# Kernel optimization log

Hardware: AMD Instinct MI355X
Metric: run time of the kernel (lower is better)

Reference implementation:

```python
import jax, jax.numpy as jnp
import numpy as np

B_SZ, SEQ, IN, HID, MEM_D, ORDER = 64, 512, 512, 1024, 8, 256
THETA = 512.0


def _legendre_ab(order, theta):
    # Continuous-time Legendre delay system (Voelker et al.):
    # A[i,j] = (2i+1)/theta * (-1 if i<j else (-1)^(i-j+1));  B[i] = (2i+1)/theta * (-1)^i
    q = jnp.arange(order, dtype=jnp.float32)
    r = (2.0 * q + 1.0) / theta
    i, j = jnp.meshgrid(q, q, indexing='ij')
    a = jnp.where(i < j, -1.0, jnp.where(((i - j) % 2) == 1, 1.0, -1.0)) * r[:, None]
    b = jnp.where((q % 2) == 0, 1.0, -1.0) * r
    # ZOH discretization with dt=1 via augmented matrix exponential
    M = jnp.zeros((order + 1, order + 1), dtype=jnp.float32)
    M = M.at[:order, :order].set(a).at[:order, order].set(b)
    Md = jax.scipy.linalg.expm(M)
    return Md[:order, :order], Md[:order, order]


def setup_inputs() -> dict:
    key = jax.random.key(0)
    ks = jax.random.split(key, 7)
    def n(k, shape, s):
        return jax.random.normal(k, shape, dtype=jnp.float32) * jnp.float32(s)
    return {
        'x':   n(ks[0], (B_SZ, SEQ, IN), 1.0),
        'e_x': n(ks[1], (MEM_D, IN), 1.0 / np.sqrt(IN)),          # lecun_uniform_-like scale
        'e_h': n(ks[2], (MEM_D, HID), 1.0 / np.sqrt(HID)),
        'e_m': jnp.zeros((MEM_D, MEM_D * ORDER), dtype=jnp.float32),  # init_em = zeros_
        'W_x': n(ks[4], (HID, IN), np.sqrt(2.0 / (HID + IN))),    # xavier_normal_
        'W_h': n(ks[5], (HID, HID), np.sqrt(2.0 / (HID + HID))),
        'W_m': n(ks[6], (HID, MEM_D * ORDER), np.sqrt(2.0 / (HID + MEM_D * ORDER))),
    }


def reference(x, e_x, e_h, e_m, W_x, W_h, W_m):
    A, Bv = _legendre_ab(ORDER, THETA)
    bsz = x.shape[0]

    def step(carry, x_t):
        h, m = carry                      # h: [B,HID], m: [B,MEM_D,ORDER]
        m_flat = m.reshape(bsz, -1)
        # u_t = e_x x_t + e_h h_{t-1} + e_m m_{t-1}  -> [B, MEM_D]
        u = x_t @ e_x.T + h @ e_h.T + m_flat @ e_m.T
        # m_t = A m_{t-1} + B u_t (per memory channel)
        m = jnp.einsum('bdo,po->bdp', m, A) + u[:, :, None] * Bv
        m_flat = m.reshape(bsz, -1)
        # h_t = tanh(W_x x_t + W_h h_{t-1} + W_m m_t)
        h = jnp.tanh(x_t @ W_x.T + h @ W_h.T + m_flat @ W_m.T)
        return (h, m), h

    h0 = jnp.zeros((bsz, HID), dtype=x.dtype)
    m0 = jnp.zeros((bsz, MEM_D, ORDER), dtype=x.dtype)
    (_, _), ys = jax.lax.scan(step, (h0, m0), jnp.swapaxes(x, 0, 1))
    return jnp.swapaxes(ys, 0, 1)          # [B, SEQ, HID]
```

## Files before the change

kernel.cpp:

```cpp
#include <hip/hip_runtime.h>
#include <cmath>
#include <vector>

#define B_SZ 64
#define SEQ 512
#define IN_D 512
#define HID 1024
#define MEM_DIM 8
#define ORD 256
#define MFLAT 2048
#define KTOT 3584
#define NH 128
#define NM 64
#define NBLK (NH + NM)
#define BAR_STRIDE 16

typedef __attribute__((ext_vector_type(8))) short short8v;
typedef __attribute__((ext_vector_type(4))) float f32x4;

__device__ __host__ inline unsigned short f2bf(float f) {
  union { float f; unsigned u; } v; v.f = f;
  unsigned r = v.u + 0x7FFF + ((v.u >> 16) & 1);
  return (unsigned short)(r >> 16);
}
__device__ __host__ inline float bf2f(unsigned short h) {
  union { unsigned u; float f; } v; v.u = ((unsigned)h) << 16;
  return v.f;
}

static void matmul_d(const double* A, const double* B, double* C, int n) {
  for (int i = 0; i < n; ++i) {
    double* Ci = C + (size_t)i * n;
    for (int j = 0; j < n; ++j) Ci[j] = 0.0;
    const double* Ai = A + (size_t)i * n;
    for (int k = 0; k < n; ++k) {
      double a = Ai[k];
      const double* Bk = B + (size_t)k * n;
      for (int j = 0; j < n; ++j) Ci[j] += a * Bk[j];
    }
  }
}

static void compute_AB_host(float* AdT, float* Anat, float* Bd) {
  const int q = ORD, n = ORD + 1;
  const double theta = 512.0;
  std::vector<double> M((size_t)n * n, 0.0);
  for (int i = 0; i < q; ++i) {
    double r = (2.0 * i + 1.0) / theta;
    for (int j = 0; j < q; ++j) {
      double v = (i < j) ? -1.0 : ((((i - j) % 2) == 1) ? 1.0 : -1.0);
      M[(size_t)i * n + j] = v * r;
    }
    M[(size_t)i * n + q] = (((i % 2) == 0) ? 1.0 : -1.0) * r;
  }
  double norm = 0.0;
  for (int j = 0; j < n; ++j) {
    double s = 0.0;
    for (int i = 0; i < n; ++i) s += fabs(M[(size_t)i * n + j]);
    if (s > norm) norm = s;
  }
  int s = 0;
  while (norm > 0.25) { norm *= 0.5; ++s; }
  double sc = ldexp(1.0, -s);
  for (size_t i = 0; i < M.size(); ++i) M[i] *= sc;
  std::vector<double> E((size_t)n * n, 0.0), P = M, T((size_t)n * n);
  for (int i = 0; i < n; ++i) E[(size_t)i * n + i] = 1.0;
  for (size_t i = 0; i < M.size(); ++i) E[i] += M[i];
  for (int k = 2; k <= 30; ++k) {
    matmul_d(P.data(), M.data(), T.data(), n);
    double inv = 1.0 / (double)k, mx = 0.0;
    for (size_t i = 0; i < T.size(); ++i) {
      T[i] *= inv;
      double a = fabs(T[i]);
      if (a > mx) mx = a;
    }
    P.swap(T);
    for (size_t i = 0; i < M.size(); ++i) E[i] += P[i];
    if (mx < 1e-19) break;
  }
  for (int it = 0; it < s; ++it) {
    matmul_d(E.data(), E.data(), T.data(), n);
    E.swap(T);
  }
  for (int p = 0; p < q; ++p) {
    for (int o = 0; o < q; ++o) {
      float v = (float)E[(size_t)p * n + o];
      AdT[(size_t)o * q + p] = v;
      Anat[(size_t)p * q + o] = v;
    }
    Bd[p] = (float)E[(size_t)p * n + q];
  }
}

__global__ __launch_bounds__(256) void k_wmb(const float* __restrict__ Wm,
                                             const float* __restrict__ Bd,
                                             float* __restrict__ WmB) {
  int i = blockIdx.x;
  int d = threadIdx.x >> 5, l = threadIdx.x & 31;
  const float* wr = Wm + (size_t)i * MFLAT + d * ORD;
  float acc = 0.f;
  #pragma unroll
  for (int j = 0; j < 8; ++j) { int p = l + 32 * j; acc += wr[p] * Bd[p]; }
  for (int off = 16; off; off >>= 1) acc += __shfl_xor(acc, off);
  if (l == 0) WmB[i * 8 + d] = acc;
}

__global__ __launch_bounds__(256) void k_gcat(
    const float* __restrict__ Wx, const float* __restrict__ Wh,
    const float* __restrict__ Wm, const float* __restrict__ Ex,
    const float* __restrict__ Eh, const float* __restrict__ Em,
    const float* __restrict__ Anat, const float* __restrict__ WmB,
    unsigned short* __restrict__ Ghi, unsigned short* __restrict__ Glo) {
  __shared__ float wm[MFLAT];
  __shared__ float wb[8];
  int i = blockIdx.x, tid = threadIdx.x;
  for (int k = tid; k < MFLAT; k += 256) wm[k] = Wm[(size_t)i * MFLAT + k];
  if (tid < 8) wb[tid] = WmB[i * 8 + tid];
  __syncthreads();
  unsigned short* grh = Ghi + (size_t)i * KTOT;
  unsigned short* grl = Glo + (size_t)i * KTOT;
  for (int c = tid; c < KTOT; c += 256) {
    float v;
    if (c < IN_D) {
      v = Wx[(size_t)i * IN_D + c];
      #pragma unroll
      for (int d = 0; d < 8; ++d) v += wb[d] * Ex[(size_t)d * IN_D + c];
    } else if (c < IN_D + HID) {
      int j = c - IN_D;
      v = Wh[(size_t)i * HID + j];
      #pragma unroll
      for (int d = 0; d < 8; ++d) v += wb[d] * Eh[(size_t)d * HID + j];
    } else {
      int cm = c - IN_D - HID;
      int dd = cm >> 8, o = cm & 255;
      v = 0.f;
      const float* wmd = wm + dd * ORD;
      for (int p = 0; p < ORD; ++p) v += wmd[p] * Anat[(size_t)p * ORD + o];
      #pragma unroll
      for (int d = 0; d < 8; ++d) v += wb[d] * Em[(size_t)d * MFLAT + cm];
    }
    unsigned short hi = f2bf(v);
    grh[c] = hi;
    grl[c] = f2bf(v - bf2f(hi));
  }
}

__device__ inline void grid_barrier(unsigned* __restrict__ arr,
                                    unsigned* __restrict__ go, unsigned ep) {
  __syncthreads();
  if (blockIdx.x == 0) {
    int tid = threadIdx.x;
    if (tid > 0 && tid < NBLK) {
      while (__hip_atomic_load(&arr[tid * BAR_STRIDE], __ATOMIC_RELAXED,
                               __HIP_MEMORY_SCOPE_AGENT) < ep) {}
    }
    __syncthreads();
    if (tid == 0)
      __hip_atomic_store(go, ep, __ATOMIC_RELEASE, __HIP_MEMORY_SCOPE_AGENT);
  } else {
    if (threadIdx.x == 0) {
      __hip_atomic_store(&arr[blockIdx.x * BAR_STRIDE], ep, __ATOMIC_RELEASE,
                         __HIP_MEMORY_SCOPE_AGENT);
      while (__hip_atomic_load(go, __ATOMIC_RELAXED,
                               __HIP_MEMORY_SCOPE_AGENT) < ep) {}
    }
  }
  if (threadIdx.x == 0)
    __builtin_amdgcn_fence(__ATOMIC_ACQUIRE, "agent");
  __syncthreads();
}

__global__ __launch_bounds__(256) void k_persist(
    const float* __restrict__ x, const float* __restrict__ Ex,
    const float* __restrict__ Eh, const float* __restrict__ Em,
    const unsigned short* __restrict__ Ghi, const unsigned short* __restrict__ Glo,
    const float* __restrict__ AdT, const float* __restrict__ Bd,
    unsigned short* __restrict__ sh0, unsigned short* __restrict__ sh1,
    unsigned short* __restrict__ sl0, unsigned short* __restrict__ sl1,
    float* __restrict__ hfp0, float* __restrict__ hfp1,
    float* __restrict__ mfp0, float* __restrict__ mfp1,
    float* __restrict__ out, unsigned* __restrict__ barArr,
    unsigned* __restrict__ barGo) {
  int tid = threadIdx.x;
  unsigned ep = 0;

  if (blockIdx.x < NH) {
    __shared__ float hx[2][64][4];
    int it = blockIdx.x & 63, bh = blockIdx.x >> 6;
    int w = tid >> 6, lane = tid & 63;
    int tw = w & 1, kh = w >> 1;
    int b0 = bh * 32 + tw * 16;
    int i0 = it * 16;
    size_t aoff = (size_t)(b0 + (lane & 15)) * KTOT + (lane >> 4) * 8;
    const unsigned short* bh_ = Ghi + (size_t)(i0 + (lane & 15)) * KTOT + (lane >> 4) * 8;
    const unsigned short* bl_ = Glo + (size_t)(i0 + (lane & 15)) * KTOT + (lane >> 4) * 8;

    grid_barrier(barArr, barGo, ++ep);

    for (int t = 0; t < SEQ; ++t) {
      const unsigned short* ah_ = ((t & 1) ? sh1 : sh0) + aoff;
      const unsigned short* al_ = ((t & 1) ? sl1 : sl0) + aoff;
      unsigned short* snh = (t & 1) ? sh0 : sh1;
      unsigned short* snl = (t & 1) ? sl0 : sl1;
      float* hn = (t & 1) ? hfp0 : hfp1;

      f32x4 ahh = {0.f,0.f,0.f,0.f}, alh = {0.f,0.f,0.f,0.f}, ahl = {0.f,0.f,0.f,0.f};
      int kbase = kh * 1792;
      #pragma unroll 4
      for (int kk = 0; kk < 56; ++kk) {
        int k = kbase + kk * 32;
        short8v avh = *(const short8v*)(ah_ + k);
        short8v avl = *(const short8v*)(al_ + k);
        short8v bvh = *(const short8v*)(bh_ + k);
        short8v bvl = *(const short8v*)(bl_ + k);
        ahh = __builtin_amdgcn_mfma_f32_16x16x32_bf16(avh, bvh, ahh, 0, 0, 0);
        alh = __builtin_amdgcn_mfma_f32_16x16x32_bf16(avl, bvh, alh, 0, 0, 0);
        ahl = __builtin_amdgcn_mfma_f32_16x16x32_bf16(avh, bvl, ahl, 0, 0, 0);
      }
      f32x4 acc = ahh + alh + ahl;
      if (kh == 1) {
        *(f32x4*)&hx[tw][lane][0] = acc;
      }
      __syncthreads();
      if (kh == 0) {
        f32x4 o4 = *(const f32x4*)&hx[tw][lane][0];
        #pragma unroll
        for (int r = 0; r < 4; ++r) {
          float v = acc[r] + o4[r];
          float hv = tanhf(v);
          int b = b0 + (lane >> 4) * 4 + r;
          int i = i0 + (lane & 15);
          hn[(size_t)b * HID + i] = hv;
          unsigned short hi = f2bf(hv);
          snh[(size_t)b * KTOT + IN_D + i] = hi;
          snl[(size_t)b * KTOT + IN_D + i] = f2bf(hv - bf2f(hi));
          __builtin_nontemporal_store(hv, &out[((size_t)b * SEQ + t) * HID + i]);
        }
      }
      grid_barrier(barArr, barGo, ++ep);
    }
  } else {
    __shared__ float sst[KTOT];
    __shared__ float part[4][MFLAT];
    __shared__ float ush[8];
    int b = blockIdx.x - NH;
    int du = tid >> 5, lu = tid & 31;
    const float* exr = Ex + (size_t)du * IN_D;
    const float* ehr = Eh + (size_t)du * HID;
    const float* emr = Em + (size_t)du * MFLAT;
    int os = tid >> 6;
    int p0 = (tid & 63) * 4;
    int dp0 = tid * 8;
    int dr = tid >> 5;
    float bdv[8];
    #pragma unroll
    for (int j = 0; j < 8; ++j) bdv[j] = Bd[(dp0 & 255) + j];

    {
      const float* xr = x + (size_t)b * SEQ * IN_D;
      for (int k = tid; k < IN_D; k += 256) {
        float xv = xr[k];
        unsigned short hi = f2bf(xv);
        sh0[(size_t)b * KTOT + k] = hi;
        sl0[(size_t)b * KTOT + k] = f2bf(xv - bf2f(hi));
      }
    }
    grid_barrier(barArr, barGo, ++ep);

    for (int t = 0; t < SEQ; ++t) {
      const float* hc = (t & 1) ? hfp1 : hfp0;
      const float* mc = (t & 1) ? mfp1 : mfp0;
      float* mn = (t & 1) ? mfp0 : mfp1;
      unsigned short* snh = (t & 1) ? sh0 : sh1;
      unsigned short* snl = (t & 1) ? sl0 : sl1;

      const float* xrow = x + ((size_t)b * SEQ + t) * IN_D;
      #pragma unroll
      for (int j = 0; j < 14; ++j) {
        int k = tid + 256 * j;
        float v;
        if (k < IN_D) v = xrow[k];
        else if (k < IN_D + HID) v = hc[(size_t)b * HID + (k - IN_D)];
        else v = mc[(size_t)b * MFLAT + (k - IN_D - HID)];
        sst[k] = v;
      }
      __syncthreads();

      float ua = 0.f;
      #pragma unroll 4
      for (int j = 0; j < 16; ++j) { int k = lu + 32 * j; ua += exr[k] * sst[k]; }
      #pragma unroll 4
      for (int j = 0; j < 32; ++j) { int k = lu + 32 * j; ua += ehr[k] * sst[IN_D + k]; }
      #pragma unroll 4
      for (int j = 0; j < 64; ++j) { int k = lu + 32 * j; ua += emr[k] * sst[IN_D + HID + k]; }
      #pragma unroll
      for (int off = 16; off; off >>= 1) ua += __shfl_xor(ua, off);
      if (lu == 0) ush[du] = ua;
      __syncthreads();

      float acc[8][4];
      #pragma unroll
      for (int d = 0; d < 8; ++d)
        acc[d][0] = acc[d][1] = acc[d][2] = acc[d][3] = 0.f;
      const float* mbase = sst + IN_D + HID;
      #pragma unroll 4
      for (int oo = 0; oo < 64; ++oo) {
        int o = os * 64 + oo;
        float4 q = *(const float4*)(AdT + (size_t)o * ORD + p0);
        #pragma unroll
        for (int d = 0; d < 8; ++d) {
          float mv = mbase[d * ORD + o];
          acc[d][0] = fmaf(q.x, mv, acc[d][0]);
          acc[d][1] = fmaf(q.y, mv, acc[d][1]);
          acc[d][2] = fmaf(q.z, mv, acc[d][2]);
          acc[d][3] = fmaf(q.w, mv, acc[d][3]);
        }
      }
      #pragma unroll
      for (int d = 0; d < 8; ++d)
        *(float4*)&part[os][d * ORD + p0] =
            make_float4(acc[d][0], acc[d][1], acc[d][2], acc[d][3]);
      __syncthreads();

      float r[8];
      float uv = ush[dr];
      #pragma unroll
      for (int j = 0; j < 8; ++j) r[j] = bdv[j] * uv;
      #pragma unroll
      for (int s = 0; s < 4; ++s) {
        float4 v0 = *(const float4*)&part[s][dp0];
        float4 v1 = *(const float4*)&part[s][dp0 + 4];
        r[0] += v0.x; r[1] += v0.y; r[2] += v0.z; r[3] += v0.w;
        r[4] += v1.x; r[5] += v1.y; r[6] += v1.z; r[7] += v1.w;
      }
      float4* mo4 = (float4*)(mn + (size_t)b * MFLAT + dp0);
      mo4[0] = make_float4(r[0], r[1], r[2], r[3]);
      mo4[1] = make_float4(r[4], r[5], r[6], r[7]);
      unsigned short ph[8], pl[8];
      #pragma unroll
      for (int j = 0; j < 8; ++j) {
        ph[j] = f2bf(r[j]);
        pl[j] = f2bf(r[j] - bf2f(ph[j]));
      }
      size_t moff = (size_t)b * KTOT + IN_D + HID + dp0;
      *(short8v*)(snh + moff) = *(short8v*)ph;
      *(short8v*)(snl + moff) = *(short8v*)pl;

      if (t + 1 < SEQ) {
        const float* xn = x + ((size_t)b * SEQ + t + 1) * IN_D;
        for (int k = tid; k < IN_D; k += 256) {
          float xv = xn[k];
          unsigned short hi = f2bf(xv);
          snh[(size_t)b * KTOT + k] = hi;
          snl[(size_t)b * KTOT + k] = f2bf(xv - bf2f(hi));
        }
      }
      grid_barrier(barArr, barGo, ++ep);
    }
  }
}

extern "C" void kernel_launch(void* const* d_in, const int* in_sizes, int n_in,
                              void* d_out, int out_size, void* d_ws, size_t ws_size,
                              hipStream_t stream) {
  const float* x  = (const float*)d_in[0];
  const float* Ex = (const float*)d_in[1];
  const float* Eh = (const float*)d_in[2];
  const float* Em = (const float*)d_in[3];
  const float* Wx = (const float*)d_in[4];
  const float* Wh = (const float*)d_in[5];
  const float* Wm = (const float*)d_in[6];
  float* out = (float*)d_out;
  float* ws = (float*)d_ws;

  float* dAnat = ws;
  float* dAdT  = dAnat + 65536;
  float* dBd   = dAdT + 65536;
  float* dWmB  = dBd + 512;
  unsigned short* dGhi = (unsigned short*)(dWmB + 8192);
  unsigned short* dGlo = dGhi + (size_t)HID * KTOT;
  unsigned short* sh0  = dGlo + (size_t)HID * KTOT;
  unsigned short* sh1  = sh0 + (size_t)B_SZ * KTOT;
  unsigned short* sl0  = sh1 + (size_t)B_SZ * KTOT;
  unsigned short* sl1  = sl0 + (size_t)B_SZ * KTOT;
  float* hfp0 = (float*)(sl1 + (size_t)B_SZ * KTOT);
  float* hfp1 = hfp0 + B_SZ * HID;
  float* mfp0 = hfp1 + B_SZ * HID;
  float* mfp1 = mfp0 + B_SZ * MFLAT;
  unsigned* barArr = (unsigned*)(mfp1 + B_SZ * MFLAT);
  unsigned* barGo  = barArr + NBLK * BAR_STRIDE;

  static float h_AdT[ORD * ORD];
  static float h_Anat[ORD * ORD];
  static float h_Bd[ORD];
  compute_AB_host(h_AdT, h_Anat, h_Bd);
  hipMemcpyAsync(dAdT,  h_AdT,  sizeof(h_AdT),  hipMemcpyHostToDevice, stream);
  hipMemcpyAsync(dAnat, h_Anat, sizeof(h_Anat), hipMemcpyHostToDevice, stream);
  hipMemcpyAsync(dBd,   h_Bd,   sizeof(h_Bd),   hipMemcpyHostToDevice, stream);

  hipMemsetAsync(sh0, 0, (size_t)B_SZ * KTOT * sizeof(unsigned short), stream);
  hipMemsetAsync(sl0, 0, (size_t)B_SZ * KTOT * sizeof(unsigned short), stream);
  hipMemsetAsync(hfp0, 0, (size_t)B_SZ * HID * sizeof(float), stream);
  hipMemsetAsync(mfp0, 0, (size_t)B_SZ * MFLAT * sizeof(float), stream);
  hipMemsetAsync(barArr, 0, (NBLK * BAR_STRIDE + 16) * sizeof(unsigned), stream);

  k_wmb<<<dim3(HID), dim3(256), 0, stream>>>(Wm, dBd, dWmB);
  k_gcat<<<dim3(HID), dim3(256), 0, stream>>>(Wx, Wh, Wm, Ex, Eh, Em, dAnat, dWmB, dGhi, dGlo);

  k_persist<<<dim3(NBLK), dim3(256), 0, stream>>>(
      x, Ex, Eh, Em, dGhi, dGlo, dAdT, dBd, sh0, sh1, sl0, sl1,
      hfp0, hfp1, mfp0, mfp1, out, barArr, barGo);
}
```

Baseline: 19.41 ms.

## Use relaxed atomic cross-block exchange and drop fp32 hidden-state buffers

The grid barrier loses its release stores and acquire fence. Cross-block shared state is now written and read with relaxed agent-scope 64-bit atomic loads and stores, which avoids cache writeback and invalidation on every step. The h-blocks pack the hi/lo bf16 hidden values through LDS into coalesced 64-bit stores. The separate fp32 h buffer is removed, so memory blocks rebuild h from the hi+lo bf16 pair. This cuts per-step barrier and store cost, but it depends on the atomics bypassing non-coherent caches. The reconstructed h also carries a small precision change. The m fp32 buffer is still read with plain loads while no acquire fence remains, which risks reading stale data.

```diff
diff --git a/kernel.cpp b/kernel.cpp
--- a/kernel.cpp
+++ b/kernel.cpp
@@ -17,6 +17,14 @@
 
 typedef __attribute__((ext_vector_type(8))) short short8v;
 typedef __attribute__((ext_vector_type(4))) float f32x4;
+typedef unsigned long long u64;
+
+__device__ inline u64 ald(const void* p) {
+  return __hip_atomic_load((const u64*)p, __ATOMIC_RELAXED, __HIP_MEMORY_SCOPE_AGENT);
+}
+__device__ inline void ast(void* p, u64 v) {
+  __hip_atomic_store((u64*)p, v, __ATOMIC_RELAXED, __HIP_MEMORY_SCOPE_AGENT);
+}
 
 __device__ __host__ inline unsigned short f2bf(float f) {
   union { float f; unsigned u; } v; v.f = f;
@@ -156,17 +164,15 @@
     }
     __syncthreads();
     if (tid == 0)
-      __hip_atomic_store(go, ep, __ATOMIC_RELEASE, __HIP_MEMORY_SCOPE_AGENT);
+      __hip_atomic_store(go, ep, __ATOMIC_RELAXED, __HIP_MEMORY_SCOPE_AGENT);
   } else {
     if (threadIdx.x == 0) {
-      __hip_atomic_store(&arr[blockIdx.x * BAR_STRIDE], ep, __ATOMIC_RELEASE,
+      __hip_atomic_store(&arr[blockIdx.x * BAR_STRIDE], ep, __ATOMIC_RELAXED,
                          __HIP_MEMORY_SCOPE_AGENT);
       while (__hip_atomic_load(go, __ATOMIC_RELAXED,
                                __HIP_MEMORY_SCOPE_AGENT) < ep) {}
     }
   }
-  if (threadIdx.x == 0)
-    __builtin_amdgcn_fence(__ATOMIC_ACQUIRE, "agent");
   __syncthreads();
 }
 
@@ -177,7 +183,6 @@
     const float* __restrict__ AdT, const float* __restrict__ Bd,
     unsigned short* __restrict__ sh0, unsigned short* __restrict__ sh1,
     unsigned short* __restrict__ sl0, unsigned short* __restrict__ sl1,
-    float* __restrict__ hfp0, float* __restrict__ hfp1,
     float* __restrict__ mfp0, float* __restrict__ mfp1,
     float* __restrict__ out, unsigned* __restrict__ barArr,
     unsigned* __restrict__ barGo) {
@@ -186,6 +191,7 @@
 
   if (blockIdx.x < NH) {
     __shared__ float hx[2][64][4];
+    __shared__ unsigned lds_pk[32][16];
     int it = blockIdx.x & 63, bh = blockIdx.x >> 6;
     int w = tid >> 6, lane = tid & 63;
     int tw = w & 1, kh = w >> 1;
@@ -202,20 +208,20 @@
       const unsigned short* al_ = ((t & 1) ? sl1 : sl0) + aoff;
       unsigned short* snh = (t & 1) ? sh0 : sh1;
       unsigned short* snl = (t & 1) ? sl0 : sl1;
-      float* hn = (t & 1) ? hfp0 : hfp1;
 
       f32x4 ahh = {0.f,0.f,0.f,0.f}, alh = {0.f,0.f,0.f,0.f}, ahl = {0.f,0.f,0.f,0.f};
       int kbase = kh * 1792;
       #pragma unroll 4
       for (int kk = 0; kk < 56; ++kk) {
         int k = kbase + kk * 32;
-        short8v avh = *(const short8v*)(ah_ + k);
-        short8v avl = *(const short8v*)(al_ + k);
+        union { u64 q[2]; short8v v; } avh, avl;
+        avh.q[0] = ald(ah_ + k);  avh.q[1] = ald(ah_ + k + 4);
+        avl.q[0] = ald(al_ + k);  avl.q[1] = ald(al_ + k + 4);
         short8v bvh = *(const short8v*)(bh_ + k);
         short8v bvl = *(const short8v*)(bl_ + k);
-        ahh = __builtin_amdgcn_mfma_f32_16x16x32_bf16(avh, bvh, ahh, 0, 0, 0);
-        alh = __builtin_amdgcn_mfma_f32_16x16x32_bf16(avl, bvh, alh, 0, 0, 0);
-        ahl = __builtin_amdgcn_mfma_f32_16x16x32_bf16(avh, bvl, ahl, 0, 0, 0);
+        ahh = __builtin_amdgcn_mfma_f32_16x16x32_bf16(avh.v, bvh, ahh, 0, 0, 0);
+        alh = __builtin_amdgcn_mfma_f32_16x16x32_bf16(avl.v, bvh, alh, 0, 0, 0);
+        ahl = __builtin_amdgcn_mfma_f32_16x16x32_bf16(avh.v, bvl, ahl, 0, 0, 0);
       }
       f32x4 acc = ahh + alh + ahl;
       if (kh == 1) {
@@ -228,14 +234,30 @@
         for (int r = 0; r < 4; ++r) {
           float v = acc[r] + o4[r];
           float hv = tanhf(v);
-          int b = b0 + (lane >> 4) * 4 + r;
+          int bl = tw * 16 + (lane >> 4) * 4 + r;
+          int b = bh * 32 + bl;
           int i = i0 + (lane & 15);
-          hn[(size_t)b * HID + i] = hv;
           unsigned short hi = f2bf(hv);
-          snh[(size_t)b * KTOT + IN_D + i] = hi;
-          snl[(size_t)b * KTOT + IN_D + i] = f2bf(hv - bf2f(hi));
+          unsigned short lo = f2bf(hv - bf2f(hi));
+          lds_pk[bl][lane & 15] = (unsigned)hi | ((unsigned)lo << 16);
           __builtin_nontemporal_store(hv, &out[((size_t)b * SEQ + t) * HID + i]);
         }
+      }
+      __syncthreads();
+      {
+        int plane = tid >> 7, row = (tid >> 2) & 31, i4 = (tid & 3) * 4;
+        unsigned w0 = lds_pk[row][i4], w1 = lds_pk[row][i4 + 1];
+        unsigned w2 = lds_pk[row][i4 + 2], w3 = lds_pk[row][i4 + 3];
+        u64 v;
+        if (plane == 0)
+          v = (u64)(w0 & 0xFFFF) | ((u64)(w1 & 0xFFFF) << 16) |
+              ((u64)(w2 & 0xFFFF) << 32) | ((u64)(w3 & 0xFFFF) << 48);
+        else
+          v = (u64)(w0 >> 16) | ((u64)(w1 >> 16) << 16) |
+              ((u64)(w2 >> 16) << 32) | ((u64)(w3 >> 16) << 48);
+        int gb = bh * 32 + row;
+        unsigned short* dst = (plane ? snl : snh) + (size_t)gb * KTOT + IN_D + i0 + i4;
+        ast(dst, v);
       }
       grid_barrier(barArr, barGo, ++ep);
     }
@@ -256,19 +278,24 @@
     #pragma unroll
     for (int j = 0; j < 8; ++j) bdv[j] = Bd[(dp0 & 255) + j];
 
-    {
+    if (tid < 128) {
       const float* xr = x + (size_t)b * SEQ * IN_D;
-      for (int k = tid; k < IN_D; k += 256) {
-        float xv = xr[k];
-        unsigned short hi = f2bf(xv);
-        sh0[(size_t)b * KTOT + k] = hi;
-        sl0[(size_t)b * KTOT + k] = f2bf(xv - bf2f(hi));
-      }
+      int k4 = tid * 4;
+      unsigned short ph[4], pl[4];
+      #pragma unroll
+      for (int j = 0; j < 4; ++j) {
+        float xv = xr[k4 + j];
+        ph[j] = f2bf(xv);
+        pl[j] = f2bf(xv - bf2f(ph[j]));
+      }
+      ast(sh0 + (size_t)b * KTOT + k4, *(u64*)ph);
+      ast(sl0 + (size_t)b * KTOT + k4, *(u64*)pl);
     }
     grid_barrier(barArr, barGo, ++ep);
 
     for (int t = 0; t < SEQ; ++t) {
-      const float* hc = (t & 1) ? hfp1 : hfp0;
+      const unsigned short* sch = (t & 1) ? sh1 : sh0;
+      const unsigned short* scl = (t & 1) ? sl1 : sl0;
       const float* mc = (t & 1) ? mfp1 : mfp0;
       float* mn = (t & 1) ? mfp0 : mfp1;
       unsigned short* snh = (t & 1) ? sh0 : sh1;
@@ -276,13 +303,27 @@
 
       const float* xrow = x + ((size_t)b * SEQ + t) * IN_D;
       #pragma unroll
-      for (int j = 0; j < 14; ++j) {
+      for (int j = 0; j < 2; ++j) {
         int k = tid + 256 * j;
-        float v;
-        if (k < IN_D) v = xrow[k];
-        else if (k < IN_D + HID) v = hc[(size_t)b * HID + (k - IN_D)];
-        else v = mc[(size_t)b * MFLAT + (k - IN_D - HID)];
-        sst[k] = v;
+        sst[k] = xrow[k];
+      }
+      {
+        int k4 = tid * 4;
+        u64 vh = ald(sch + (size_t)b * KTOT + IN_D + k4);
+        u64 vl = ald(scl + (size_t)b * KTOT + IN_D + k4);
+        #pragma unroll
+        for (int j = 0; j < 4; ++j)
+          sst[IN_D + k4 + j] = bf2f((unsigned short)(vh >> (16 * j))) +
+                               bf2f((unsigned short)(vl >> (16 * j)));
+      }
+      {
+        const float4* mc4 = (const float4*)(mc + (size_t)b * MFLAT);
+        float4* sst4 = (float4*)(sst + IN_D + HID);
+        #pragma unroll
+        for (int j = 0; j < 2; ++j) {
+          int g = tid + 256 * j;
+          sst4[g] = mc4[g];
+        }
       }
       __syncthreads();
 
@@ -343,17 +384,23 @@
         pl[j] = f2bf(r[j] - bf2f(ph[j]));
       }
       size_t moff = (size_t)b * KTOT + IN_D + HID + dp0;
-      *(short8v*)(snh + moff) = *(short8v*)ph;
-      *(short8v*)(snl + moff) = *(short8v*)pl;
-
-      if (t + 1 < SEQ) {
+      ast(snh + moff,     ((u64*)ph)[0]);
+      ast(snh + moff + 4, ((u64*)ph)[1]);
+      ast(snl + moff,     ((u64*)pl)[0]);
+      ast(snl + moff + 4, ((u64*)pl)[1]);
+
+      if (t + 1 < SEQ && tid < 128) {
         const float* xn = x + ((size_t)b * SEQ + t + 1) * IN_D;
-        for (int k = tid; k < IN_D; k += 256) {
-          float xv = xn[k];
-          unsigned short hi = f2bf(xv);
-          snh[(size_t)b * KTOT + k] = hi;
-          snl[(size_t)b * KTOT + k] = f2bf(xv - bf2f(hi));
+        int k4 = tid * 4;
+        unsigned short qh[4], ql[4];
+        #pragma unroll
+        for (int j = 0; j < 4; ++j) {
+          float xv = xn[k4 + j];
+          qh[j] = f2bf(xv);
+          ql[j] = f2bf(xv - bf2f(qh[j]));
         }
+        ast(snh + (size_t)b * KTOT + k4, *(u64*)qh);
+        ast(snl + (size_t)b * KTOT + k4, *(u64*)ql);
       }
       grid_barrier(barArr, barGo, ++ep);
     }
@@ -383,9 +430,7 @@
   unsigned short* sh1  = sh0 + (size_t)B_SZ * KTOT;
   unsigned short* sl0  = sh1 + (size_t)B_SZ * KTOT;
   unsigned short* sl1  = sl0 + (size_t)B_SZ * KTOT;
-  float* hfp0 = (float*)(sl1 + (size_t)B_SZ * KTOT);
-  float* hfp1 = hfp0 + B_SZ * HID;
-  float* mfp0 = hfp1 + B_SZ * HID;
+  float* mfp0 = (float*)(sl1 + (size_t)B_SZ * KTOT);
   float* mfp1 = mfp0 + B_SZ * MFLAT;
   unsigned* barArr = (unsigned*)(mfp1 + B_SZ * MFLAT);
   unsigned* barGo  = barArr + NBLK * BAR_STRIDE;
@@ -400,7 +445,6 @@
 
   hipMemsetAsync(sh0, 0, (size_t)B_SZ * KTOT * sizeof(unsigned short), stream);
   hipMemsetAsync(sl0, 0, (size_t)B_SZ * KTOT * sizeof(unsigned short), stream);
-  hipMemsetAsync(hfp0, 0, (size_t)B_SZ * HID * sizeof(float), stream);
   hipMemsetAsync(mfp0, 0, (size_t)B_SZ * MFLAT * sizeof(float), stream);
   hipMemsetAsync(barArr, 0, (NBLK * BAR_STRIDE + 16) * sizeof(unsigned), stream);
 
@@ -409,5 +453,5 @@
 
   k_persist<<<dim3(NBLK), dim3(256), 0, stream>>>(
       x, Ex, Eh, Em, dGhi, dGlo, dAdT, dBd, sh0, sh1, sl0, sl1,
-      hfp0, hfp1, mfp0, mfp1, out, barArr, barGo);
-}
+      mfp0, mfp1, out, barArr, barGo);
+}
```

Result: slower. 21.34 ms (+10.0%).
